# Kernel tuning notes

Hardware: AMD Instinct MI355X
Metric: run time of the kernel (lower is better)

Reference implementation:

```python
import jax, jax.numpy as jnp
import numpy as np


def _structure_constants():
    # Octonion multiplication table: e_i * e_j = sum_k C[i,j,k] e_k.
    # e0 is the real unit; imaginary triples follow the standard Fano-plane
    # convention (Baez): e_a e_b = e_c for the cyclic triples below.
    C = np.zeros((8, 8, 8), dtype=np.float32)
    C[0, 0, 0] = 1.0
    for i in range(1, 8):
        C[0, i, i] = 1.0   # 1 * e_i = e_i
        C[i, 0, i] = 1.0   # e_i * 1 = e_i
        C[i, i, 0] = -1.0  # e_i * e_i = -1
    triples = [(1, 2, 3), (1, 4, 5), (1, 7, 6), (2, 4, 6), (2, 5, 7), (3, 4, 7), (3, 6, 5)]
    for (a, b, c) in triples:
        for (p, q, r) in ((a, b, c), (b, c, a), (c, a, b)):
            C[p, q, r] = 1.0
            C[q, p, r] = -1.0
    return C


_C = _structure_constants()

IN_FEATURES = 64
OUT_FEATURES = 64
BATCH = (16, 4096)


def setup_inputs() -> dict:
    key = jax.random.key(0)
    kx, kw, kb = jax.random.split(key, 3)
    x = jax.random.normal(kx, (*BATCH, IN_FEATURES, 8), dtype=jnp.float32)
    # 8 octonion-component weight matrices, stacked: [8, out, in]
    scale = 1.0 / np.sqrt(IN_FEATURES * 8)
    W = jax.random.normal(kw, (8, OUT_FEATURES, IN_FEATURES), dtype=jnp.float32) * scale
    b = jax.random.normal(kb, (OUT_FEATURES, 8), dtype=jnp.float32) * 0.01
    return {"x": x, "W": W, "b": b}


def reference(x, W, b):
    # out[..., o, k] = sum_{i,j,f} C[i,j,k] * W[i,o,f] * x[..., f, j] + b[o, k]
    # Fold the sparse structure constants into one block weight, then a single
    # contraction (the fused-GEMM formulation of the original 64-linear loop).
    C = jnp.asarray(_C, dtype=x.dtype)
    Wbig = jnp.einsum('iof,ijk->okfj', W, C)        # [out, 8, in, 8]
    out = jnp.einsum('...fj,okfj->...ok', x, Wbig)  # [..., out, 8]
    return out + b
```

## Files before the change

kernel.cpp:

```cpp
#include <hip/hip_runtime.h>
#include <hip/hip_bf16.h>

typedef __attribute__((ext_vector_type(8))) short short8;
typedef __attribute__((ext_vector_type(4))) float f32x4;

#define BM 128
#define BN 128
#define BK 64
#define LDST 72

static __device__ __forceinline__ unsigned short f2bf(float f) {
    union { __hip_bfloat16 h; unsigned short u; } cv;
    cv.h = __float2bfloat16(f);
    return cv.u;
}

__global__ __launch_bounds__(256) void build_wbig(const float* __restrict__ W,
                                                  unsigned short* __restrict__ Wbig) {
    __shared__ float C[8][8][8];
    const int t = threadIdx.x;
    for (int i = t; i < 512; i += 256) ((float*)C)[i] = 0.0f;
    __syncthreads();
    if (t == 0) {
        C[0][0][0] = 1.0f;
        for (int i = 1; i < 8; ++i) { C[0][i][i] = 1.0f; C[i][0][i] = 1.0f; C[i][i][0] = -1.0f; }
        const int tr[7][3] = {{1,2,3},{1,4,5},{1,7,6},{2,4,6},{2,5,7},{3,4,7},{3,6,5}};
        for (int q = 0; q < 7; ++q) {
            const int a = tr[q][0], b = tr[q][1], c = tr[q][2];
            const int p[3][3] = {{a,b,c},{b,c,a},{c,a,b}};
            for (int u = 0; u < 3; ++u) {
                C[p[u][0]][p[u][1]][p[u][2]] = 1.0f;
                C[p[u][1]][p[u][0]][p[u][2]] = -1.0f;
            }
        }
    }
    __syncthreads();
    const int e = blockIdx.x * 256 + t;
    const int m = e >> 9, kk = e & 511;
    const int o = m >> 3, k = m & 7, f = kk >> 3, j = kk & 7;
    float s = 0.0f;
#pragma unroll
    for (int i = 0; i < 8; ++i) s += C[i][j][k] * W[i * 4096 + o * 64 + f];
    Wbig[e] = f2bf(s);
}

__global__ __launch_bounds__(256) void oct_gemm(const float* __restrict__ X,
                                                const unsigned short* __restrict__ Wbig,
                                                const float* __restrict__ Bias,
                                                float* __restrict__ Out) {
    __shared__ unsigned short As[BM * LDST];
    __shared__ unsigned short Bs[BN * LDST];

    const int bid   = blockIdx.x;
    const int xcd   = bid & 7;
    const int ix    = bid >> 3;
    const int ntile = xcd * 64 + (ix >> 2);
    const int mtile = ix & 3;
    const int rowBase = ntile * BM;
    const int colBase = mtile * BN;

    const int t    = threadIdx.x;
    const int lane = t & 63;
    const int wave = t >> 6;
    const int wr   = wave >> 1, wc = wave & 1;

    f32x4 acc[4][4];
#pragma unroll
    for (int i = 0; i < 4; ++i)
#pragma unroll
        for (int j = 0; j < 4; ++j) acc[i][j] = (f32x4){0.f, 0.f, 0.f, 0.f};

    const int srow = t >> 3;
    const int scol = (t & 7) * 8;

    for (int kt = 0; kt < 512; kt += BK) {
#pragma unroll
        for (int l = 0; l < 4; ++l) {
            const int r = l * 32 + srow;
            const float* src = X + (size_t)(rowBase + r) * 512 + kt + scol;
            f32x4 v0 = *reinterpret_cast<const f32x4*>(src);
            f32x4 v1 = *reinterpret_cast<const f32x4*>(src + 4);
            short8 p;
            p[0] = (short)f2bf(v0[0]); p[1] = (short)f2bf(v0[1]);
            p[2] = (short)f2bf(v0[2]); p[3] = (short)f2bf(v0[3]);
            p[4] = (short)f2bf(v1[0]); p[5] = (short)f2bf(v1[1]);
            p[6] = (short)f2bf(v1[2]); p[7] = (short)f2bf(v1[3]);
            *reinterpret_cast<short8*>(&As[r * LDST + scol]) = p;
        }
#pragma unroll
        for (int l = 0; l < 4; ++l) {
            const int r = l * 32 + srow;
            short8 v = *reinterpret_cast<const short8*>(Wbig + (size_t)(colBase + r) * 512 + kt + scol);
            *reinterpret_cast<short8*>(&Bs[r * LDST + scol]) = v;
        }
        __syncthreads();

#pragma unroll
        for (int kk = 0; kk < 2; ++kk) {
            const int kb = kk * 32 + (lane >> 4) * 8;
            short8 a[4], b[4];
#pragma unroll
            for (int mi = 0; mi < 4; ++mi)
                a[mi] = *reinterpret_cast<const short8*>(&As[(wr * 64 + mi * 16 + (lane & 15)) * LDST + kb]);
#pragma unroll
            for (int ni = 0; ni < 4; ++ni)
                b[ni] = *reinterpret_cast<const short8*>(&Bs[(wc * 64 + ni * 16 + (lane & 15)) * LDST + kb]);
#pragma unroll
            for (int mi = 0; mi < 4; ++mi)
#pragma unroll
                for (int ni = 0; ni < 4; ++ni)
                    acc[mi][ni] = __builtin_amdgcn_mfma_f32_16x16x32_bf16(a[mi], b[ni], acc[mi][ni], 0, 0, 0);
        }
        __syncthreads();
    }

    float bv[4];
#pragma unroll
    for (int ni = 0; ni < 4; ++ni) bv[ni] = Bias[colBase + wc * 64 + ni * 16 + (lane & 15)];
#pragma unroll
    for (int mi = 0; mi < 4; ++mi) {
        const int row0 = rowBase + wr * 64 + mi * 16 + (lane >> 4) * 4;
#pragma unroll
        for (int ni = 0; ni < 4; ++ni) {
            const int col = colBase + wc * 64 + ni * 16 + (lane & 15);
#pragma unroll
            for (int r = 0; r < 4; ++r)
                Out[(size_t)(row0 + r) * 512 + col] = acc[mi][ni][r] + bv[ni];
        }
    }
}

extern "C" void kernel_launch(void* const* d_in, const int* in_sizes, int n_in,
                              void* d_out, int out_size, void* d_ws, size_t ws_size,
                              hipStream_t stream) {
    const float* x = (const float*)d_in[0];
    const float* W = (const float*)d_in[1];
    const float* b = (const float*)d_in[2];
    float* out = (float*)d_out;
    unsigned short* Wbig = (unsigned short*)d_ws;

    build_wbig<<<1024, 256, 0, stream>>>(W, Wbig);
    oct_gemm<<<2048, 256, 0, stream>>>(x, Wbig, b, out);
}
```

Baseline: 76.97 us.

## Double-buffer A tile in LDS, load B fragments directly from global

Restructures the GEMM main loop so the next X tile is prefetched into registers while MFMAs run on the current LDS buffer, using two A buffers and one barrier per k-step. Wbig fragments are read straight from global memory (L2-resident) into registers, dropping the B shared-memory tile. Accumulators are seeded with the bias, and outputs are written with nontemporal stores. This raises register pressure and relies on the cache for B reuse.

Result: slower. 109.6 us (+42.4%).

```diff
diff --git a/kernel.cpp b/kernel.cpp
--- a/kernel.cpp
+++ b/kernel.cpp
@@ -8,6 +8,7 @@
 #define BN 128
 #define BK 64
 #define LDST 72
+#define NKT 8
 
 static __device__ __forceinline__ unsigned short f2bf(float f) {
     union { __hip_bfloat16 h; unsigned short u; } cv;
@@ -48,8 +49,7 @@
                                                 const unsigned short* __restrict__ Wbig,
                                                 const float* __restrict__ Bias,
                                                 float* __restrict__ Out) {
-    __shared__ unsigned short As[BM * LDST];
-    __shared__ unsigned short Bs[BN * LDST];
+    __shared__ unsigned short As[2][BM * LDST];
 
     const int bid   = blockIdx.x;
     const int xcd   = bid & 7;
@@ -64,59 +64,79 @@
     const int wave = t >> 6;
     const int wr   = wave >> 1, wc = wave & 1;
 
-    f32x4 acc[4][4];
-#pragma unroll
-    for (int i = 0; i < 4; ++i)
-#pragma unroll
-        for (int j = 0; j < 4; ++j) acc[i][j] = (f32x4){0.f, 0.f, 0.f, 0.f};
-
     const int srow = t >> 3;
     const int scol = (t & 7) * 8;
 
-    for (int kt = 0; kt < 512; kt += BK) {
+    const float* Xrow = X + (size_t)(rowBase + srow) * 512 + scol;
+
+    f32x4 v[8];
+
+#define ISSUE_A(KT) do { _Pragma("unroll") \
+    for (int l = 0; l < 4; ++l) { \
+        const float* src = Xrow + (size_t)(l * 32) * 512 + (KT); \
+        v[2*l]   = *reinterpret_cast<const f32x4*>(src); \
+        v[2*l+1] = *reinterpret_cast<const f32x4*>(src + 4); \
+    } } while (0)
+
+#define WRITE_A(BUF) do { _Pragma("unroll") \
+    for (int l = 0; l < 4; ++l) { \
+        short8 p; \
+        p[0]=(short)f2bf(v[2*l][0]);   p[1]=(short)f2bf(v[2*l][1]); \
+        p[2]=(short)f2bf(v[2*l][2]);   p[3]=(short)f2bf(v[2*l][3]); \
+        p[4]=(short)f2bf(v[2*l+1][0]); p[5]=(short)f2bf(v[2*l+1][1]); \
+        p[6]=(short)f2bf(v[2*l+1][2]); p[7]=(short)f2bf(v[2*l+1][3]); \
+        *reinterpret_cast<short8*>(&As[BUF][(l*32 + srow) * LDST + scol]) = p; \
+    } } while (0)
+
+    f32x4 acc[4][4];
 #pragma unroll
-        for (int l = 0; l < 4; ++l) {
-            const int r = l * 32 + srow;
-            const float* src = X + (size_t)(rowBase + r) * 512 + kt + scol;
-            f32x4 v0 = *reinterpret_cast<const f32x4*>(src);
-            f32x4 v1 = *reinterpret_cast<const f32x4*>(src + 4);
-            short8 p;
-            p[0] = (short)f2bf(v0[0]); p[1] = (short)f2bf(v0[1]);
-            p[2] = (short)f2bf(v0[2]); p[3] = (short)f2bf(v0[3]);
-            p[4] = (short)f2bf(v1[0]); p[5] = (short)f2bf(v1[1]);
-            p[6] = (short)f2bf(v1[2]); p[7] = (short)f2bf(v1[3]);
-            *reinterpret_cast<short8*>(&As[r * LDST + scol]) = p;
-        }
+    for (int ni = 0; ni < 4; ++ni) {
+        const float bv = Bias[colBase + wc * 64 + ni * 16 + (lane & 15)];
 #pragma unroll
-        for (int l = 0; l < 4; ++l) {
-            const int r = l * 32 + srow;
-            short8 v = *reinterpret_cast<const short8*>(Wbig + (size_t)(colBase + r) * 512 + kt + scol);
-            *reinterpret_cast<short8*>(&Bs[r * LDST + scol]) = v;
-        }
-        __syncthreads();
+        for (int mi = 0; mi < 4; ++mi) acc[mi][ni] = (f32x4){bv, bv, bv, bv};
+    }
+
+    const unsigned short* Bb = Wbig + (size_t)(colBase + wc * 64 + (lane & 15)) * 512
+                                    + (lane >> 4) * 8;
+
+    ISSUE_A(0);
+    WRITE_A(0);
+    __syncthreads();
+
+    int cur = 0;
+#pragma unroll
+    for (int kt = 0; kt < NKT; ++kt) {
+        if (kt + 1 < NKT) ISSUE_A((kt + 1) * BK);
+
+        short8 b[2][4];
+#pragma unroll
+        for (int kk = 0; kk < 2; ++kk)
+#pragma unroll
+            for (int ni = 0; ni < 4; ++ni)
+                b[kk][ni] = *reinterpret_cast<const short8*>(Bb + (size_t)ni * (16 * 512)
+                                                             + kt * BK + kk * 32);
 
 #pragma unroll
         for (int kk = 0; kk < 2; ++kk) {
             const int kb = kk * 32 + (lane >> 4) * 8;
-            short8 a[4], b[4];
+            short8 a[4];
 #pragma unroll
             for (int mi = 0; mi < 4; ++mi)
-                a[mi] = *reinterpret_cast<const short8*>(&As[(wr * 64 + mi * 16 + (lane & 15)) * LDST + kb]);
-#pragma unroll
-            for (int ni = 0; ni < 4; ++ni)
-                b[ni] = *reinterpret_cast<const short8*>(&Bs[(wc * 64 + ni * 16 + (lane & 15)) * LDST + kb]);
+                a[mi] = *reinterpret_cast<const short8*>(
+                    &As[cur][(wr * 64 + mi * 16 + (lane & 15)) * LDST + kb]);
 #pragma unroll
             for (int mi = 0; mi < 4; ++mi)
 #pragma unroll
                 for (int ni = 0; ni < 4; ++ni)
-                    acc[mi][ni] = __builtin_amdgcn_mfma_f32_16x16x32_bf16(a[mi], b[ni], acc[mi][ni], 0, 0, 0);
+                    acc[mi][ni] = __builtin_amdgcn_mfma_f32_16x16x32_bf16(
+                        a[mi], b[kk][ni], acc[mi][ni], 0, 0, 0);
         }
+
+        if (kt + 1 < NKT) WRITE_A(cur ^ 1);
         __syncthreads();
+        cur ^= 1;
     }
 
-    float bv[4];
-#pragma unroll
-    for (int ni = 0; ni < 4; ++ni) bv[ni] = Bias[colBase + wc * 64 + ni * 16 + (lane & 15)];
 #pragma unroll
     for (int mi = 0; mi < 4; ++mi) {
         const int row0 = rowBase + wr * 64 + mi * 16 + (lane >> 4) * 4;
@@ -125,9 +145,12 @@
             const int col = colBase + wc * 64 + ni * 16 + (lane & 15);
 #pragma unroll
             for (int r = 0; r < 4; ++r)
-                Out[(size_t)(row0 + r) * 512 + col] = acc[mi][ni][r] + bv[ni];
+                __builtin_nontemporal_store(acc[mi][ni][r],
+                                            &Out[(size_t)(row0 + r) * 512 + col]);
         }
     }
+#undef ISSUE_A
+#undef WRITE_A
 }
 
 extern "C" void kernel_launch(void* const* d_in, const int* in_sizes, int n_in,
```

## Keep Wbig resident in registers and stream X tiles through double-buffered LDS

Applied to the files above, without the earlier changes.

Restructures the GEMM as a persistent kernel: 256 blocks of 1024 threads each loop over 4 row chunks of 64 rows. Each of the 16 waves holds its 32-column slice of Wbig entirely in registers, so B is never staged through shared memory. X is prefetched three k-steps ahead into registers, converted to bf16, and written into a double-buffered LDS tile. Bias is folded into the accumulator initialisation. This removes repeated B traffic and per-tile B LDS work, in exchange for very high register pressure (32 short8 per lane) and lower occupancy.

New measurement: 126.2 us. +64.0%, slower.

```diff
diff --git a/kernel.cpp b/kernel.cpp
--- a/kernel.cpp
+++ b/kernel.cpp
@@ -2,12 +2,11 @@
 #include <hip/hip_bf16.h>
 
 typedef __attribute__((ext_vector_type(8))) short short8;
+typedef __attribute__((ext_vector_type(4))) short short4v;
 typedef __attribute__((ext_vector_type(4))) float f32x4;
 
-#define BM 128
-#define BN 128
-#define BK 64
 #define LDST 72
+#define NCH 4
 
 static __device__ __forceinline__ unsigned short f2bf(float f) {
     union { __hip_bfloat16 h; unsigned short u; } cv;
@@ -44,89 +43,102 @@
     Wbig[e] = f2bf(s);
 }
 
-__global__ __launch_bounds__(256) void oct_gemm(const float* __restrict__ X,
-                                                const unsigned short* __restrict__ Wbig,
-                                                const float* __restrict__ Bias,
-                                                float* __restrict__ Out) {
-    __shared__ unsigned short As[BM * LDST];
-    __shared__ unsigned short Bs[BN * LDST];
-
-    const int bid   = blockIdx.x;
-    const int xcd   = bid & 7;
-    const int ix    = bid >> 3;
-    const int ntile = xcd * 64 + (ix >> 2);
-    const int mtile = ix & 3;
-    const int rowBase = ntile * BM;
-    const int colBase = mtile * BN;
+__global__ __launch_bounds__(1024, 4) void oct_gemm(const float* __restrict__ X,
+                                                    const unsigned short* __restrict__ Wbig,
+                                                    const float* __restrict__ Bias,
+                                                    float* __restrict__ Out) {
+    __shared__ unsigned short As[2][64 * LDST];
 
     const int t    = threadIdx.x;
     const int lane = t & 63;
-    const int wave = t >> 6;
-    const int wr   = wave >> 1, wc = wave & 1;
+    const int w    = t >> 6;
+    const int l15  = lane & 15;
+    const int l4   = lane >> 4;
 
-    f32x4 acc[4][4];
+    short8 breg[2][16];
+    {
+        const unsigned short* bp = Wbig + (size_t)(w * 32 + l15) * 512 + l4 * 8;
 #pragma unroll
-    for (int i = 0; i < 4; ++i)
+        for (int ni = 0; ni < 2; ++ni)
 #pragma unroll
-        for (int j = 0; j < 4; ++j) acc[i][j] = (f32x4){0.f, 0.f, 0.f, 0.f};
+            for (int ks = 0; ks < 16; ++ks)
+                breg[ni][ks] = *reinterpret_cast<const short8*>(bp + (size_t)ni * 16 * 512 + ks * 32);
+    }
 
-    const int srow = t >> 3;
-    const int scol = (t & 7) * 8;
+    const float bv0 = Bias[w * 32 + l15];
+    const float bv1 = Bias[w * 32 + 16 + l15];
 
-    for (int kt = 0; kt < 512; kt += BK) {
+    const int srow  = t >> 4;
+    const int scol4 = (t & 15) * 4;
+
+    for (int ch = 0; ch < NCH; ++ch) {
+        const int rowBase = ((ch << 8) + (int)blockIdx.x) << 6;
+        const float* Xp = X + (size_t)(rowBase + srow) * 512 + scol4;
+
+        f32x4 va[3];
+
+#define LD(SLOT, KT) va[SLOT] = *reinterpret_cast<const f32x4*>(Xp + (KT))
+#define WRITE(BUF, SLOT) do { \
+        short4v p; \
+        p[0] = (short)f2bf(va[SLOT][0]); p[1] = (short)f2bf(va[SLOT][1]); \
+        p[2] = (short)f2bf(va[SLOT][2]); p[3] = (short)f2bf(va[SLOT][3]); \
+        *reinterpret_cast<short4v*>(&As[BUF][srow * LDST + scol4]) = p; \
+    } while (0)
+#define BARRIER() do { \
+        asm volatile("s_waitcnt lgkmcnt(0)" ::: "memory"); \
+        __builtin_amdgcn_s_barrier(); \
+    } while (0)
+
+        f32x4 acc[4][2];
 #pragma unroll
-        for (int l = 0; l < 4; ++l) {
-            const int r = l * 32 + srow;
-            const float* src = X + (size_t)(rowBase + r) * 512 + kt + scol;
-            f32x4 v0 = *reinterpret_cast<const f32x4*>(src);
-            f32x4 v1 = *reinterpret_cast<const f32x4*>(src + 4);
-            short8 p;
-            p[0] = (short)f2bf(v0[0]); p[1] = (short)f2bf(v0[1]);
-            p[2] = (short)f2bf(v0[2]); p[3] = (short)f2bf(v0[3]);
-            p[4] = (short)f2bf(v1[0]); p[5] = (short)f2bf(v1[1]);
-            p[6] = (short)f2bf(v1[2]); p[7] = (short)f2bf(v1[3]);
-            *reinterpret_cast<short8*>(&As[r * LDST + scol]) = p;
+        for (int mi = 0; mi < 4; ++mi) {
+            acc[mi][0] = (f32x4){bv0, bv0, bv0, bv0};
+            acc[mi][1] = (f32x4){bv1, bv1, bv1, bv1};
         }
-#pragma unroll
-        for (int l = 0; l < 4; ++l) {
-            const int r = l * 32 + srow;
-            short8 v = *reinterpret_cast<const short8*>(Wbig + (size_t)(colBase + r) * 512 + kt + scol);
-            *reinterpret_cast<short8*>(&Bs[r * LDST + scol]) = v;
-        }
-        __syncthreads();
+
+        LD(0, 0); LD(1, 64); LD(2, 128);
+        WRITE(0, 0);
+        BARRIER();
 
 #pragma unroll
-        for (int kk = 0; kk < 2; ++kk) {
-            const int kb = kk * 32 + (lane >> 4) * 8;
-            short8 a[4], b[4];
+        for (int it = 0; it < 8; ++it) {
+            if (it <= 4) LD(it % 3, (it + 3) * 64);
+
 #pragma unroll
-            for (int mi = 0; mi < 4; ++mi)
-                a[mi] = *reinterpret_cast<const short8*>(&As[(wr * 64 + mi * 16 + (lane & 15)) * LDST + kb]);
+            for (int kk = 0; kk < 2; ++kk) {
+                const int kb = kk * 32 + l4 * 8;
+                short8 a[4];
 #pragma unroll
-            for (int ni = 0; ni < 4; ++ni)
-                b[ni] = *reinterpret_cast<const short8*>(&Bs[(wc * 64 + ni * 16 + (lane & 15)) * LDST + kb]);
+                for (int mi = 0; mi < 4; ++mi)
+                    a[mi] = *reinterpret_cast<const short8*>(
+                        &As[it & 1][(mi * 16 + l15) * LDST + kb]);
 #pragma unroll
-            for (int mi = 0; mi < 4; ++mi)
+                for (int mi = 0; mi < 4; ++mi) {
+                    acc[mi][0] = __builtin_amdgcn_mfma_f32_16x16x32_bf16(
+                        a[mi], breg[0][it * 2 + kk], acc[mi][0], 0, 0, 0);
+                    acc[mi][1] = __builtin_amdgcn_mfma_f32_16x16x32_bf16(
+                        a[mi], breg[1][it * 2 + kk], acc[mi][1], 0, 0, 0);
+                }
+            }
+
+            if (it < 7) WRITE((it + 1) & 1, (it + 1) % 3);
+            BARRIER();
+        }
+
 #pragma unroll
-                for (int ni = 0; ni < 4; ++ni)
-                    acc[mi][ni] = __builtin_amdgcn_mfma_f32_16x16x32_bf16(a[mi], b[ni], acc[mi][ni], 0, 0, 0);
+        for (int mi = 0; mi < 4; ++mi) {
+            const int row0 = rowBase + mi * 16 + l4 * 4;
+#pragma unroll
+            for (int ni = 0; ni < 2; ++ni) {
+                const int col = w * 32 + ni * 16 + l15;
+#pragma unroll
+                for (int r = 0; r < 4; ++r)
+                    Out[(size_t)(row0 + r) * 512 + col] = acc[mi][ni][r];
+            }
         }
-        __syncthreads();
-    }
-
-    float bv[4];
-#pragma unroll
-    for (int ni = 0; ni < 4; ++ni) bv[ni] = Bias[colBase + wc * 64 + ni * 16 + (lane & 15)];
-#pragma unroll
-    for (int mi = 0; mi < 4; ++mi) {
-        const int row0 = rowBase + wr * 64 + mi * 16 + (lane >> 4) * 4;
-#pragma unroll
-        for (int ni = 0; ni < 4; ++ni) {
-            const int col = colBase + wc * 64 + ni * 16 + (lane & 15);
-#pragma unroll
-            for (int r = 0; r < 4; ++r)
-                Out[(size_t)(row0 + r) * 512 + col] = acc[mi][ni][r] + bv[ni];
-        }
+#undef LD
+#undef WRITE
+#undef BARRIER
     }
 }
 
@@ -140,5 +152,5 @@
     unsigned short* Wbig = (unsigned short*)d_ws;
 
     build_wbig<<<1024, 256, 0, stream>>>(W, Wbig);
-    oct_gemm<<<2048, 256, 0, stream>>>(x, Wbig, b, out);
+    oct_gemm<<<256, 1024, 0, stream>>>(x, Wbig, b, out);
 }
```
